# Kernel tuning notes

Hardware: AMD Instinct MI355X
Metric: run time of the kernel (lower is better)

## Reference

```python
import jax, jax.numpy as jnp
import numpy as np

N = 100000          # nodes
E = 3_200_000       # edges (avg degree 32)
F_IN = 1433
H1, C1 = 8, 8       # conv1: 8 heads x 8 channels -> 64 concat
H2, C2 = 1, 7       # conv2: 1 head x 7 classes
NEG_SLOPE = 0.2


def setup_inputs() -> dict:
    key = jax.random.key(0)
    ks = jax.random.split(key, 10)
    x = jax.random.normal(ks[0], (N, F_IN), dtype=jnp.float32)
    edge_index = jax.random.randint(ks[1], (2, E), 0, N, dtype=jnp.int64)
    s1 = 1.0 / np.sqrt(F_IN)
    s2 = 1.0 / np.sqrt(H1 * C1)
    return {
        "x": x,
        "edge_index": edge_index,
        "W1": jax.random.normal(ks[2], (F_IN, H1 * C1), dtype=jnp.float32) * s1,
        "att_src1": jax.random.normal(ks[3], (H1, C1), dtype=jnp.float32) * s2,
        "att_dst1": jax.random.normal(ks[4], (H1, C1), dtype=jnp.float32) * s2,
        "b1": jnp.zeros((H1 * C1,), dtype=jnp.float32),
        "W2": jax.random.normal(ks[5], (H1 * C1, H2 * C2), dtype=jnp.float32) * s2,
        "att_src2": jax.random.normal(ks[6], (H2, C2), dtype=jnp.float32),
        "att_dst2": jax.random.normal(ks[7], (H2, C2), dtype=jnp.float32),
        "b2": jnp.zeros((H2 * C2,), dtype=jnp.float32),
    }


def gat_conv(x, src, dst, W, att_src, att_dst, b, heads, ch):
    # x: [N, F_in]; src/dst: [E'] (self-loops already appended)
    h = (x @ W).reshape(N, heads, ch)                     # [N, H, C]
    a_src = jnp.einsum('nhc,hc->nh', h, att_src)          # [N, H]
    a_dst = jnp.einsum('nhc,hc->nh', h, att_dst)
    e = a_src[src] + a_dst[dst]                           # [E', H]
    e = jax.nn.leaky_relu(e, NEG_SLOPE)
    # segment softmax over incoming edges of each dst node
    m = jax.ops.segment_max(e, dst, num_segments=N)       # [N, H]
    w = jnp.exp(e - m[dst])
    denom = jax.ops.segment_sum(w, dst, num_segments=N)   # [N, H]
    alpha = w / denom[dst]                                # [E', H]
    msg = alpha[:, :, None] * h[src]                      # [E', H, C]
    out = jax.ops.segment_sum(msg, dst, num_segments=N)   # [N, H, C]
    return out.reshape(N, heads * ch) + b


def reference(x, edge_index, W1, att_src1, att_dst1, b1, W2, att_src2, att_dst2, b2):
    loops = jnp.arange(N, dtype=edge_index.dtype)
    src = jnp.concatenate([edge_index[0], loops])
    dst = jnp.concatenate([edge_index[1], loops])
    # eval mode: all dropout layers are identity
    h = gat_conv(x, src, dst, W1, att_src1, att_dst1, b1, H1, C1)   # [N, 64]
    h = jax.nn.elu(h)
    h = gat_conv(h, src, dst, W2, att_src2, att_dst2, b2, H2, C2)   # [N, 7]
    return jax.nn.log_softmax(h, axis=1)
```

## Files before the change

### kernel.cpp

```cpp
#include <hip/hip_runtime.h>
#include <hip/hip_bf16.h>
#include <math.h>

#define NN 100000
#define EE 3200000
#define ET (EE + NN)
#define FIN 1433
#define KPAD 1440
#define NT 45
#define F1 64
#define F2 7
#define G1B 782
#define CAP 128
#define BINS 200
#define SB1 256
#define CH_E 12891
#define NB4 196
#define A1B 3125

typedef __attribute__((ext_vector_type(8))) short short8;
typedef __attribute__((ext_vector_type(4))) float f32x4;
typedef __attribute__((address_space(3))) unsigned int u32_lds;
typedef __attribute__((address_space(1))) const unsigned int u32_glb;

static __device__ __forceinline__ unsigned short f2bf(float f) {
  __hip_bfloat16 h = __float2bfloat16(f);
  return *reinterpret_cast<unsigned short*>(&h);
}
static __device__ __forceinline__ float bf2f(unsigned short u) {
  return __uint_as_float((unsigned int)u << 16);
}

__global__ __launch_bounds__(256) void k_prep(const float* __restrict__ W1,
                                              unsigned short* __restrict__ WT) {
  int i = blockIdx.x * 256 + threadIdx.x;
  if (i < F1 * KPAD) {
    int c = i / KPAD, k = i - c * KPAD;
    WT[i] = f2bf((k < FIN) ? W1[k * F1 + c] : 0.f);
  }
}

#define BM 128
#define TILEA 16384
#define TILEB 4096
#define BUFB (TILEA + TILEB)

__global__ __launch_bounds__(256) void k_gemm1(const float* __restrict__ X,
                                               const unsigned short* __restrict__ WT,
                                               unsigned short* __restrict__ Hb) {
  __shared__ __align__(16) char smem[2 * BUFB];
  const int tid = threadIdx.x;
  const int lane = tid & 63;
  const int wid = tid >> 6;
  const int row0 = blockIdx.x * BM;
  const int wr = (wid >> 1) * 64;
  const int wc = (wid & 1) * 32;
  const int l15 = lane & 15, l4 = lane >> 4;

  const int lrq = tid >> 3;
  const int mq = tid & 7;
  const char* Xb = (const char*)X;
  size_t aoff[4];
#pragma unroll
  for (int q = 0; q < 4; ++q) {
    int lr = q * 32 + lrq;
    int gr = row0 + lr; if (gr >= NN) gr = NN - 1;
    int c = mq ^ (lr & 7);
    aoff[q] = (size_t)gr * (FIN * 4) + (size_t)c * 16;
  }
  const unsigned short* bsrc =
      WT + (tid >> 2) * KPAD + (((tid & 3) ^ ((tid >> 3) & 3)) << 3);

  f32x4 acc[4][2];
#pragma unroll
  for (int a = 0; a < 4; ++a)
#pragma unroll
    for (int b = 0; b < 2; ++b) acc[a][b] = 0.f;

  auto gstage = [&](int k0, char* buf) {
#pragma unroll
    for (int q = 0; q < 4; ++q) {
      __builtin_amdgcn_global_load_lds(
          (u32_glb*)(Xb + aoff[q] + (size_t)k0 * 4),
          (u32_lds*)(buf + q * 4096 + wid * 1024), 16, 0, 0);
    }
  };

  gstage(0, smem);
  {
    short8 b0 = *(const short8*)(bsrc + 0);
    *(short8*)(smem + TILEA + tid * 16) = b0;
  }
  __syncthreads();

  int cur = 0;
  for (int t = 0; t < NT; ++t) {
    char* buf = smem + cur * BUFB;
    char* nbuf = smem + (cur ^ 1) * BUFB;
    const bool have_next = (t + 1 < NT);
    const bool tail = (t + 1 == NT - 1);
    short8 bnext;
    f32x4 atail[4];
    if (have_next) {
      if (!tail) {
        gstage((t + 1) * 32, nbuf);
      } else {
#pragma unroll
        for (int q = 0; q < 4; ++q) {
          int lr = q * 32 + lrq;
          int gr = row0 + lr; if (gr >= NN) gr = NN - 1;
          int c = mq ^ (lr & 7);
          int kb = (NT - 1) * 32 + c * 4;
          const float* xp = X + (size_t)gr * FIN + kb;
#pragma unroll
          for (int j = 0; j < 4; ++j)
            atail[q][j] = (kb + j < FIN) ? xp[j] : 0.f;
        }
      }
      bnext = *(const short8*)(bsrc + (t + 1) * 32);
    }

    short8 af[4], bf[2];
    const int sz = l15 & 7;
#pragma unroll
    for (int fr = 0; fr < 4; ++fr) {
      int r = wr + fr * 16 + l15;
      f32x4 a0 = *(const f32x4*)(buf + r * 128 + ((2 * l4) ^ sz) * 16);
      f32x4 a1 = *(const f32x4*)(buf + r * 128 + ((2 * l4 + 1) ^ sz) * 16);
      short8 v;
#pragma unroll
      for (int j = 0; j < 4; ++j) {
        v[j] = (short)f2bf(a0[j]);
        v[4 + j] = (short)f2bf(a1[j]);
      }
      af[fr] = v;
    }
#pragma unroll
    for (int fc = 0; fc < 2; ++fc) {
      int c = wc + fc * 16 + l15;
      int jp = l4 ^ ((c >> 1) & 3);
      bf[fc] = *(const short8*)(buf + TILEA + c * 64 + jp * 16);
    }
#pragma unroll
    for (int fr = 0; fr < 4; ++fr)
#pragma unroll
      for (int fc = 0; fc < 2; ++fc)
        acc[fr][fc] = __builtin_amdgcn_mfma_f32_16x16x32_bf16(
            af[fr], bf[fc], acc[fr][fc], 0, 0, 0);

    if (have_next) {
      if (tail) {
#pragma unroll
        for (int q = 0; q < 4; ++q)
          *(f32x4*)(nbuf + (q * 32 + lrq) * 128 + mq * 16) = atail[q];
      }
      *(short8*)(nbuf + TILEA + tid * 16) = bnext;
    }
    __syncthreads();
    cur ^= 1;
  }

#pragma unroll
  for (int fr = 0; fr < 4; ++fr) {
    int rbase = row0 + wr + fr * 16 + l4 * 4;
#pragma unroll
    for (int q = 0; q < 4; ++q) {
      int r = rbase + q;
      if (r < NN) {
#pragma unroll
        for (int fc = 0; fc < 2; ++fc)
          Hb[(size_t)r * F1 + wc + fc * 16 + l15] = f2bf(acc[fr][fc][q]);
      }
    }
  }
}

__global__ __launch_bounds__(256) void k_hist(const int* __restrict__ ei,
                                              int* __restrict__ histM) {
  __shared__ int hist[BINS];
  const int b = blockIdx.x;
  for (int i = threadIdx.x; i < BINS; i += 256) hist[i] = 0;
  __syncthreads();
  const int e0 = b * CH_E, e1 = min(e0 + CH_E, ET);
  for (int e = e0 + threadIdx.x; e < e1; e += 256) {
    int dst = (e < EE) ? ei[EE + e] : (e - EE);
    atomicAdd(&hist[dst >> 9], 1);
  }
  __syncthreads();
  for (int i = threadIdx.x; i < BINS; i += 256) histM[b * BINS + i] = hist[i];
}

__global__ __launch_bounds__(256) void k_scanM(int* __restrict__ histM,
                                               int* __restrict__ binS,
                                               int* __restrict__ binE) {
  __shared__ int s[256];
  const int t = threadIdx.x;
  int total = 0;
  if (t < BINS)
    for (int b = 0; b < SB1; ++b) total += histM[b * BINS + t];
  s[t] = total;
  __syncthreads();
  for (int off = 1; off < 256; off <<= 1) {
    int v = s[t];
    int u = (t >= off) ? s[t - off] : 0;
    __syncthreads();
    s[t] = v + u;
    __syncthreads();
  }
  if (t < BINS) {
    int run = s[t] - total;
    binS[t] = run;
    for (int b = 0; b < SB1; ++b) {
      int h = histM[b * BINS + t];
      histM[b * BINS + t] = run;
      run += h;
    }
    binE[t] = run;
  }
}

__global__ __launch_bounds__(256) void k_bin(const int* __restrict__ ei,
                                             const int* __restrict__ histM,
                                             unsigned int* __restrict__ binned) {
  __shared__ int cur[BINS];
  const int b = blockIdx.x;
  for (int i = threadIdx.x; i < BINS; i += 256) cur[i] = histM[b * BINS + i];
  __syncthreads();
  const int e0 = b * CH_E, e1 = min(e0 + CH_E, ET);
  for (int e = e0 + threadIdx.x; e < e1; e += 256) {
    int dst = (e < EE) ? ei[EE + e] : (e - EE);
    int src = (e < EE) ? ei[e] : dst;
    int pos = atomicAdd(&cur[dst >> 9], 1);
    binned[pos] = ((unsigned)(dst & 511) << 17) | (unsigned)src;
  }
}

__global__ __launch_bounds__(256) void k_fuse2(const unsigned short* __restrict__ Hb,
                                               const float* __restrict__ attS,
                                               const float* __restrict__ attD,
                                               float* __restrict__ aS,
                                               float* __restrict__ aD,
                                               const unsigned int* __restrict__ binned,
                                               const int* __restrict__ binS,
                                               const int* __restrict__ binE,
                                               int* __restrict__ cnt,
                                               int* __restrict__ csr) {
  if (blockIdx.x >= A1B) {
    __shared__ int lcnt[512];
    const int g = blockIdx.x - A1B;
    for (int i = threadIdx.x; i < 512; i += 256) lcnt[i] = 0;
    __syncthreads();
    const int s0 = binS[g], s1 = binE[g];
    const int nbase = g << 9;
    for (int i = s0 + threadIdx.x; i < s1; i += 256) {
      unsigned v = binned[i];
      int ld = v >> 17;
      int src = (int)(v & 0x1FFFFu);
      int pos = atomicAdd(&lcnt[ld], 1);
      csr[((size_t)(nbase + ld) << 7) + pos] = src;
    }
    __syncthreads();
    for (int i = threadIdx.x; i < 512; i += 256) {
      int n = nbase + i;
      if (n < NN) cnt[n] = lcnt[i];
    }
    return;
  }
  __shared__ float s_s[64], s_d[64];
  if (threadIdx.x < 64) { s_s[threadIdx.x] = attS[threadIdx.x]; s_d[threadIdx.x] = attD[threadIdx.x]; }
  __syncthreads();
  int idx = blockIdx.x * 256 + threadIdx.x;
  int n = idx >> 3, h = idx & 7;
  if (n >= NN) return;
  short8 v8 = *(const short8*)(Hb + (size_t)n * 64 + h * 8);
  float ss = 0.f, dd = 0.f;
#pragma unroll
  for (int c = 0; c < 8; ++c) {
    float v = bf2f((unsigned short)v8[c]);
    ss = fmaf(v, s_s[h * 8 + c], ss);
    dd = fmaf(v, s_d[h * 8 + c], dd);
  }
  aS[n * 8 + h] = ss;
  aD[n * 8 + h] = dd;
}

__global__ __launch_bounds__(256) void k_agg1(const unsigned short* __restrict__ Hb,
                                              const float* __restrict__ aS,
                                              const float* __restrict__ aD,
                                              const int* __restrict__ cnt,
                                              const int* __restrict__ csr,
                                              const float* __restrict__ b1,
                                              const float* __restrict__ W2,
                                              const float* __restrict__ s2,
                                              const float* __restrict__ d2,
                                              unsigned short* __restrict__ H2b,
                                              float* __restrict__ aD2) {
  __shared__ float s_w2[448];
  __shared__ float s_ss[7], s_dd[7];
  __shared__ float s_b1[64];
  for (int i = threadIdx.x; i < 448; i += 256) s_w2[i] = W2[i];
  if (threadIdx.x < 7) { s_ss[threadIdx.x] = s2[threadIdx.x]; s_dd[threadIdx.x] = d2[threadIdx.x]; }
  if (threadIdx.x < 64) s_b1[threadIdx.x] = b1[threadIdx.x];
  __syncthreads();

  const int wv = threadIdx.x >> 6, lane = threadIdx.x & 63;
  const int n = blockIdx.x * 4 + wv;
  if (n >= NN) return;
  const int eg = lane >> 3, q = lane & 7;
  const float adv = aD[n * 8 + q];
  const int beg = n << 7;
  const int deg = cnt[n];
  float acc[8] = {};
  float den = 0.f;
#pragma unroll 2
  for (int i = eg; i < deg; i += 8) {
    int s = csr[beg + i];
    float e = aS[s * 8 + q] + adv;
    e = (e > 0.f) ? e : 0.2f * e;
    float w = __expf(e);
    den += w;
    short8 hv = *(const short8*)(Hb + (size_t)s * 64 + q * 8);
#pragma unroll
    for (int c = 0; c < 8; ++c)
      acc[c] = fmaf(w, bf2f((unsigned short)hv[c]), acc[c]);
  }
#pragma unroll
  for (int off = 8; off < 64; off <<= 1) {
    den += __shfl_xor(den, off, 64);
#pragma unroll
    for (int c = 0; c < 8; ++c) acc[c] += __shfl_xor(acc[c], off, 64);
  }
  if (eg == 0) {
    float inv = 1.f / den;
    float v[8];
#pragma unroll
    for (int c = 0; c < 8; ++c) {
      float t = acc[c] * inv + s_b1[q * 8 + c];
      v[c] = (t > 0.f) ? t : (__expf(t) - 1.f);
    }
    float p[7] = {};
#pragma unroll
    for (int c = 0; c < 8; ++c) {
      const float* wr = &s_w2[(q * 8 + c) * 7];
#pragma unroll
      for (int j = 0; j < 7; ++j) p[j] = fmaf(v[c], wr[j], p[j]);
    }
#pragma unroll
    for (int off = 1; off < 8; off <<= 1) {
#pragma unroll
      for (int j = 0; j < 7; ++j) p[j] += __shfl_xor(p[j], off, 64);
    }
    if (q == 0) {
      float s = 0.f, d = 0.f;
      short8 row;
#pragma unroll
      for (int j = 0; j < 7; ++j) {
        row[j] = (short)f2bf(p[j]);
        s = fmaf(p[j], s_ss[j], s);
        d = fmaf(p[j], s_dd[j], d);
      }
      row[7] = (short)f2bf(s);
      *(short8*)(H2b + (size_t)n * 8) = row;
      aD2[n] = d;
    }
  }
}

__global__ __launch_bounds__(256) void k_agg2(const unsigned short* __restrict__ H2b,
                                              const float* __restrict__ aD2,
                                              const int* __restrict__ cnt,
                                              const int* __restrict__ csr,
                                              const float* __restrict__ b2,
                                              float* __restrict__ out) {
  const int wv = threadIdx.x >> 6, lane = threadIdx.x & 63;
  const int n = blockIdx.x * 4 + wv;
  if (n >= NN) return;
  const float adv = aD2[n];
  const int beg = n << 7;
  const int deg = cnt[n];
  float acc[7] = {};
  float den = 0.f;
  for (int j = lane; j < deg; j += 64) {
    int s = csr[beg + j];
    short8 hv = *(const short8*)(H2b + (size_t)s * 8);
    float e = bf2f((unsigned short)hv[7]) + adv;
    e = (e > 0.f) ? e : 0.2f * e;
    float wgt = __expf(e);
    den += wgt;
#pragma unroll
    for (int c = 0; c < 7; ++c)
      acc[c] = fmaf(wgt, bf2f((unsigned short)hv[c]), acc[c]);
  }
#pragma unroll
  for (int off = 32; off > 0; off >>= 1) {
    den += __shfl_xor(den, off, 64);
#pragma unroll
    for (int c = 0; c < 7; ++c) acc[c] += __shfl_xor(acc[c], off, 64);
  }
  if (lane == 0) {
    float inv = 1.f / den;
    float v[7];
    float m = -1e30f;
#pragma unroll
    for (int c = 0; c < 7; ++c) { v[c] = acc[c] * inv + b2[c]; m = fmaxf(m, v[c]); }
    float se = 0.f;
#pragma unroll
    for (int c = 0; c < 7; ++c) se += __expf(v[c] - m);
    float lse = m + __logf(se);
#pragma unroll
    for (int c = 0; c < 7; ++c) out[n * 7 + c] = v[c] - lse;
  }
}

extern "C" void kernel_launch(void* const* d_in, const int* in_sizes, int n_in,
                              void* d_out, int out_size, void* d_ws, size_t ws_size,
                              hipStream_t stream) {
  const float* x   = (const float*)d_in[0];
  const int*   ei  = (const int*)d_in[1];
  const float* W1  = (const float*)d_in[2];
  const float* as1 = (const float*)d_in[3];
  const float* ad1 = (const float*)d_in[4];
  const float* b1  = (const float*)d_in[5];
  const float* W2  = (const float*)d_in[6];
  const float* as2 = (const float*)d_in[7];
  const float* ad2 = (const float*)d_in[8];
  const float* b2  = (const float*)d_in[9];
  float* out = (float*)d_out;

  char* ws = (char*)d_ws;
  size_t off = 0;
  auto alloc = [&](size_t bytes) {
    void* p = ws + off;
    off += (bytes + 255) & ~(size_t)255;
    return p;
  };
  unsigned short* h1b = (unsigned short*)alloc((size_t)NN * 64 * 2);
  float* sc1    = (float*)alloc((size_t)NN * 8 * 4);
  float* dc1    = (float*)alloc((size_t)NN * 8 * 4);
  unsigned short* h2b = (unsigned short*)alloc((size_t)NN * 8 * 2);
  float* dc2    = (float*)alloc((size_t)NN * 4);
  int*   cnt    = (int*)alloc((size_t)NN * 4);
  int*   csr    = (int*)alloc((size_t)NN * CAP * 4);
  int*   histM  = (int*)alloc((size_t)SB1 * BINS * 4);
  int*   binS   = (int*)alloc((size_t)BINS * 4);
  int*   binE   = (int*)alloc((size_t)BINS * 4);
  unsigned int* binned = (unsigned int*)alloc((size_t)ET * 4);
  unsigned short* w1t = (unsigned short*)alloc((size_t)F1 * KPAD * 2);

  k_prep<<<(F1 * KPAD + 255) / 256, 256, 0, stream>>>(W1, w1t);

  k_gemm1<<<G1B, 256, 0, stream>>>(x, w1t, h1b);

  k_hist<<<SB1, 256, 0, stream>>>(ei, histM);

  k_scanM<<<1, 256, 0, stream>>>(histM, binS, binE);

  k_bin<<<SB1, 256, 0, stream>>>(ei, histM, binned);

  k_fuse2<<<A1B + NB4, 256, 0, stream>>>(h1b, as1, ad1, sc1, dc1,
                                         binned, binS, binE, cnt, csr);

  k_agg1<<<(NN + 3) / 4, 256, 0, stream>>>(h1b, sc1, dc1, cnt, csr, b1,
                                           W2, as2, ad2, h2b, dc2);

  k_agg2<<<(NN + 3) / 4, 256, 0, stream>>>(h2b, dc2, cnt, csr, b2, out);
}
```

Measured before the change: 451.2 us.

## Replace LDS double-buffered GEMM1 with direct-register per-wave MFMA kernel

Rewrites the first-layer X@W1 GEMM to drop the LDS staging, async global-to-LDS loads and per-tile barriers. Each wave now computes 16 rows by 64 columns, loading X rows straight into registers and reading the bf16 W1 fragments from global/L2. The grid doubles to 64-row blocks. This removes synchronisation and LDS traffic and relies on memory-level parallelism from more waves, at the cost of uncoalesced strided X loads and no reuse of the B fragments across rows through LDS.

```diff
diff --git a/kernel.cpp b/kernel.cpp
--- a/kernel.cpp
+++ b/kernel.cpp
@@ -10,7 +10,7 @@
 #define NT 45
 #define F1 64
 #define F2 7
-#define G1B 782
+#define G1B 1563
 #define CAP 128
 #define BINS 200
 #define SB1 256
@@ -20,8 +20,6 @@
 
 typedef __attribute__((ext_vector_type(8))) short short8;
 typedef __attribute__((ext_vector_type(4))) float f32x4;
-typedef __attribute__((address_space(3))) unsigned int u32_lds;
-typedef __attribute__((address_space(1))) const unsigned int u32_glb;
 
 static __device__ __forceinline__ unsigned short f2bf(float f) {
   __hip_bfloat16 h = __float2bfloat16(f);
@@ -40,139 +38,53 @@
   }
 }
 
-#define BM 128
-#define TILEA 16384
-#define TILEB 4096
-#define BUFB (TILEA + TILEB)
-
 __global__ __launch_bounds__(256) void k_gemm1(const float* __restrict__ X,
                                                const unsigned short* __restrict__ WT,
                                                unsigned short* __restrict__ Hb) {
-  __shared__ __align__(16) char smem[2 * BUFB];
-  const int tid = threadIdx.x;
-  const int lane = tid & 63;
-  const int wid = tid >> 6;
-  const int row0 = blockIdx.x * BM;
-  const int wr = (wid >> 1) * 64;
-  const int wc = (wid & 1) * 32;
+  const int lane = threadIdx.x & 63, w = threadIdx.x >> 6;
+  const int r0 = blockIdx.x * 64 + w * 16;
+  if (r0 >= NN) return;
   const int l15 = lane & 15, l4 = lane >> 4;
 
-  const int lrq = tid >> 3;
-  const int mq = tid & 7;
-  const char* Xb = (const char*)X;
-  size_t aoff[4];
-#pragma unroll
-  for (int q = 0; q < 4; ++q) {
-    int lr = q * 32 + lrq;
-    int gr = row0 + lr; if (gr >= NN) gr = NN - 1;
-    int c = mq ^ (lr & 7);
-    aoff[q] = (size_t)gr * (FIN * 4) + (size_t)c * 16;
-  }
-  const unsigned short* bsrc =
-      WT + (tid >> 2) * KPAD + (((tid & 3) ^ ((tid >> 3) & 3)) << 3);
-
-  f32x4 acc[4][2];
-#pragma unroll
-  for (int a = 0; a < 4; ++a)
-#pragma unroll
-    for (int b = 0; b < 2; ++b) acc[a][b] = 0.f;
-
-  auto gstage = [&](int k0, char* buf) {
-#pragma unroll
-    for (int q = 0; q < 4; ++q) {
-      __builtin_amdgcn_global_load_lds(
-          (u32_glb*)(Xb + aoff[q] + (size_t)k0 * 4),
-          (u32_lds*)(buf + q * 4096 + wid * 1024), 16, 0, 0);
-    }
-  };
-
-  gstage(0, smem);
-  {
-    short8 b0 = *(const short8*)(bsrc + 0);
-    *(short8*)(smem + TILEA + tid * 16) = b0;
-  }
-  __syncthreads();
-
-  int cur = 0;
+  const float* xlane = X + (size_t)(r0 + l15) * FIN + l4 * 8;
+
+  f32x4 acc[4];
+#pragma unroll
+  for (int fc = 0; fc < 4; ++fc) acc[fc] = 0.f;
+
+#pragma unroll 2
   for (int t = 0; t < NT; ++t) {
-    char* buf = smem + cur * BUFB;
-    char* nbuf = smem + (cur ^ 1) * BUFB;
-    const bool have_next = (t + 1 < NT);
-    const bool tail = (t + 1 == NT - 1);
-    short8 bnext;
-    f32x4 atail[4];
-    if (have_next) {
-      if (!tail) {
-        gstage((t + 1) * 32, nbuf);
-      } else {
-#pragma unroll
-        for (int q = 0; q < 4; ++q) {
-          int lr = q * 32 + lrq;
-          int gr = row0 + lr; if (gr >= NN) gr = NN - 1;
-          int c = mq ^ (lr & 7);
-          int kb = (NT - 1) * 32 + c * 4;
-          const float* xp = X + (size_t)gr * FIN + kb;
-#pragma unroll
-          for (int j = 0; j < 4; ++j)
-            atail[q][j] = (kb + j < FIN) ? xp[j] : 0.f;
-        }
+    const int k0 = t * 32;
+    short8 a;
+    if (t < NT - 1) {
+      float lo[4], hi[4];
+      __builtin_memcpy(lo, xlane + k0, 16);
+      __builtin_memcpy(hi, xlane + k0 + 4, 16);
+#pragma unroll
+      for (int j = 0; j < 4; ++j) {
+        a[j] = (short)f2bf(lo[j]);
+        a[4 + j] = (short)f2bf(hi[j]);
       }
-      bnext = *(const short8*)(bsrc + (t + 1) * 32);
-    }
-
-    short8 af[4], bf[2];
-    const int sz = l15 & 7;
-#pragma unroll
-    for (int fr = 0; fr < 4; ++fr) {
-      int r = wr + fr * 16 + l15;
-      f32x4 a0 = *(const f32x4*)(buf + r * 128 + ((2 * l4) ^ sz) * 16);
-      f32x4 a1 = *(const f32x4*)(buf + r * 128 + ((2 * l4 + 1) ^ sz) * 16);
-      short8 v;
-#pragma unroll
-      for (int j = 0; j < 4; ++j) {
-        v[j] = (short)f2bf(a0[j]);
-        v[4 + j] = (short)f2bf(a1[j]);
+    } else {
+#pragma unroll
+      for (int e = 0; e < 8; ++e) {
+        int k = k0 + l4 * 8 + e;
+        a[e] = (k < FIN) ? (short)f2bf(xlane[k0 + e]) : (short)0;
       }
-      af[fr] = v;
-    }
-#pragma unroll
-    for (int fc = 0; fc < 2; ++fc) {
-      int c = wc + fc * 16 + l15;
-      int jp = l4 ^ ((c >> 1) & 3);
-      bf[fc] = *(const short8*)(buf + TILEA + c * 64 + jp * 16);
-    }
-#pragma unroll
-    for (int fr = 0; fr < 4; ++fr)
-#pragma unroll
-      for (int fc = 0; fc < 2; ++fc)
-        acc[fr][fc] = __builtin_amdgcn_mfma_f32_16x16x32_bf16(
-            af[fr], bf[fc], acc[fr][fc], 0, 0, 0);
-
-    if (have_next) {
-      if (tail) {
-#pragma unroll
-        for (int q = 0; q < 4; ++q)
-          *(f32x4*)(nbuf + (q * 32 + lrq) * 128 + mq * 16) = atail[q];
-      }
-      *(short8*)(nbuf + TILEA + tid * 16) = bnext;
-    }
-    __syncthreads();
-    cur ^= 1;
-  }
-
-#pragma unroll
-  for (int fr = 0; fr < 4; ++fr) {
-    int rbase = row0 + wr + fr * 16 + l4 * 4;
-#pragma unroll
-    for (int q = 0; q < 4; ++q) {
-      int r = rbase + q;
-      if (r < NN) {
-#pragma unroll
-        for (int fc = 0; fc < 2; ++fc)
-          Hb[(size_t)r * F1 + wc + fc * 16 + l15] = f2bf(acc[fr][fc][q]);
-      }
-    }
-  }
+    }
+#pragma unroll
+    for (int fc = 0; fc < 4; ++fc) {
+      int c = fc * 16 + l15;
+      short8 b = *(const short8*)(WT + (size_t)c * KPAD + k0 + l4 * 8);
+      acc[fc] = __builtin_amdgcn_mfma_f32_16x16x32_bf16(a, b, acc[fc], 0, 0, 0);
+    }
+  }
+
+#pragma unroll
+  for (int fc = 0; fc < 4; ++fc)
+#pragma unroll
+    for (int j = 0; j < 4; ++j)
+      Hb[(size_t)(r0 + l4 * 4 + j) * F1 + fc * 16 + l15] = f2bf(acc[fc][j]);
 }
 
 __global__ __launch_bounds__(256) void k_hist(const int* __restrict__ ei,
```

New measurement: 504.9 us. 1.12x slower.
